# Kernel optimization log

Measured on AMD Instinct MI355X. Metric: run time of the kernel, lower is better.

Reference implementation:

```python
import jax, jax.numpy as jnp
import numpy as np

BETA = 1.0  # init beta


def l2norm(x, eps=1e-12):
    # matches torch F.normalize(dim=-1)
    n = jnp.sqrt(jnp.sum(x * x, axis=-1, keepdims=True))
    return x / jnp.maximum(n, eps)


def setup_inputs() -> dict:
    key = jax.random.key(0)
    k1, k2 = jax.random.split(key)
    B, T, D, N = 8, 2048, 256, 8192
    z = jax.random.normal(k1, (B, T, D), dtype=jnp.float32)
    # EMA codebook weight (buffer, not trained by grad); l2-normalized as the
    # norm-EMA update keeps it on the unit sphere.
    weight = l2norm(jax.random.normal(k2, (N, D), dtype=jnp.float32))
    return {"z": z, "weight": weight}


def reference(z, weight):
    # z: (B, T, D); weight: (N, D)
    z = l2norm(z)
    zf = z.reshape(-1, z.shape[-1])  # (BT, D)
    # squared L2 distances via expansion: |z|^2 + |w|^2 - 2 z.w
    d = (
        jnp.sum(zf * zf, axis=1, keepdims=True)
        + jnp.sum(weight * weight, axis=1)
        - 2.0 * jnp.einsum("bd,nd->bn", zf, weight)
    )  # (BT, N)
    encoding_indices = jnp.argmin(d, axis=1)  # (BT,)
    z_q = weight[encoding_indices].reshape(z.shape)  # (B, T, D)
    # commitment loss: beta * mse(stop_grad(z_q), z)
    loss = BETA * jnp.mean((jax.lax.stop_gradient(z_q) - z) ** 2)
    # straight-through estimator
    z_q = z + jax.lax.stop_gradient(z_q - z)
    encoding_indices = encoding_indices.reshape(z.shape[:-1])  # (B, T)
    return z_q, loss, encoding_indices
```

## Files before the change

### kernel.cpp

```cpp
#include <hip/hip_runtime.h>
#include <float.h>
#include <math.h>


#define BT_ 16384
#define D_  256
#define N_  8192
#define BETA_ 1.0f

#define BM 128
#define BN 256
#define NKT 8
#define NTILES 32

typedef __attribute__((ext_vector_type(8))) _Float16 f16x8;
typedef __attribute__((ext_vector_type(4))) float f32x4;

__device__ __forceinline__ void gld16(void* lds, const void* g) {
  __builtin_amdgcn_global_load_lds(
      (const __attribute__((address_space(1))) void*)g,
      (__attribute__((address_space(3))) void*)lds, 16, 0, 0);
}

__device__ __forceinline__ unsigned short f2h(float x) {
  _Float16 h = (_Float16)x;
  return __builtin_bit_cast(unsigned short, h);
}
__device__ __forceinline__ float h2f(unsigned short u) {
  return (float)__builtin_bit_cast(_Float16, u);
}
__device__ __forceinline__ unsigned ford(float f) {
  unsigned b = __float_as_uint(f);
  return (b & 0x80000000u) ? ~b : (b | 0x80000000u);
}

__global__ __launch_bounds__(256) void k_prep(const float* __restrict__ z,
                                              const float* __restrict__ w,
                                              float* __restrict__ zn,
                                              ushort* __restrict__ Acat,
                                              float* __restrict__ rl,
                                              float* __restrict__ wn2,
                                              ushort* __restrict__ Bcat) {
  const int b    = blockIdx.x;
  const int lane = threadIdx.x & 63;
  if (b < BT_ / 4) {
    const int row = b * 4 + (threadIdx.x >> 6);
    float4 v = *(reinterpret_cast<const float4*>(z) + (size_t)row * 64 + lane);
    float s = v.x * v.x + v.y * v.y + v.z * v.z + v.w * v.w;
#pragma unroll
    for (int o = 32; o > 0; o >>= 1) s += __shfl_xor(s, o, 64);
    float dn = fmaxf(sqrtf(s), 1e-12f);
    v.x /= dn; v.y /= dn; v.z /= dn; v.w /= dn;
    *(reinterpret_cast<float4*>(zn) + (size_t)row * 64 + lane) = v;
    ushort4 h = make_ushort4(f2h(v.x), f2h(v.y), f2h(v.z), f2h(v.w));
    float lx = v.x - h2f(h.x), ly = v.y - h2f(h.y);
    float lz = v.z - h2f(h.z), lw = v.w - h2f(h.w);
    float s2 = lx * lx + ly * ly + lz * lz + lw * lw;
#pragma unroll
    for (int o = 32; o > 0; o >>= 1) s2 += __shfl_xor(s2, o, 64);
    if (lane == 0) rl[row] = sqrtf(s2);
    reinterpret_cast<ushort4*>(Acat)[(size_t)row * 64 + lane] = h;
  } else {
    const int row = (b - BT_ / 4) * 4 + (threadIdx.x >> 6);
    float4 v = *(reinterpret_cast<const float4*>(w) + (size_t)row * 64 + lane);
    float s = v.x * v.x + v.y * v.y + v.z * v.z + v.w * v.w;
#pragma unroll
    for (int o = 32; o > 0; o >>= 1) s += __shfl_xor(s, o, 64);
    if (lane == 0) wn2[row] = s;
    ushort4 h  = make_ushort4(f2h(v.x), f2h(v.y), f2h(v.z), f2h(v.w));
    ushort4 lo = make_ushort4(f2h(v.x - h2f(h.x)), f2h(v.y - h2f(h.y)),
                              f2h(v.z - h2f(h.z)), f2h(v.w - h2f(h.w)));
    ushort4* B4 = reinterpret_cast<ushort4*>(Bcat);
    size_t rb = (size_t)row * 128 + lane;
    B4[rb]      = h;
    B4[rb + 64] = lo;
  }
}

__global__ __launch_bounds__(512, 4) void k_coarse(const ushort* __restrict__ Acat,
                                                   const ushort* __restrict__ Bcat,
                                                   const float* __restrict__ wn2,
                                                   float* __restrict__ tm,
                                                   float* __restrict__ ts,
                                                   int* __restrict__ ti,
                                                   float* __restrict__ tm2) {
  extern __shared__ char smem[];

  const int tid = threadIdx.x;
  const int l   = tid & 63;
  const int wv  = tid >> 6;
  const int wr  = wv >> 2;
  const int wc  = wv & 3;
  const int bid  = blockIdx.x;
  const int xcd  = bid & 7;
  const int q    = bid >> 3;
  const int chnk = q >> 5, wq = q & 31;
  const int rt   = xcd * 16 + (chnk >> 3) * 8 + (wq >> 2);
  const int ct   = (chnk & 7) * 4 + (wq & 3);
  const int row0 = rt * BM;
  const int col0 = ct * BN;

  const int sgr = ((l & 3) ^ ((l >> 3) & 3)) * 16;
  const char* gsrc[4];
  unsigned    ldst[4];
#pragma unroll
  for (int s = 0; s < 4; ++s) {
    int u = wv * 4 + s;
    gsrc[s] = (const char*)Bcat + (size_t)(col0 + (u & 15) * 16 + (l >> 2)) * 1024 +
              (u >> 4) * 512 + sgr;
    ldst[s] = u * 1024;
  }
#define STAGE(t)                                                               \
  do {                                                                         \
    char* _b = smem + ((t) & 1) * 32768;                                       \
    _Pragma("unroll")                                                          \
    for (int s = 0; s < 4; ++s) gld16(_b + ldst[s], gsrc[s] + (size_t)(t) * 64); \
  } while (0)

  const int lA = l & 15;
  const ushort* aB = Acat + (size_t)(row0 + wr * 64 + lA) * 256 + (l >> 4) * 8;
#define LOADA(t)                                                               \
  do {                                                                         \
    _Pragma("unroll")                                                          \
    for (int i = 0; i < 4; ++i)                                                \
      af[i] = *(const f16x8*)(aB + i * 4096 + (t) * 32);                       \
  } while (0)

  const int gk = (l >> 4) ^ ((lA >> 1) & 3);
  const unsigned bOff = (unsigned)((wc * 64 + lA) * 64 + gk * 16);

  f32x4 acc[4][4];
#pragma unroll
  for (int i = 0; i < 4; ++i)
#pragma unroll
    for (int j = 0; j < 4; ++j) acc[i][j] = (f32x4){0.f, 0.f, 0.f, 0.f};

  f16x8 af[4];
  STAGE(0);
  LOADA(0);

#pragma unroll
  for (int t = 0; t < NKT; ++t) {
    char* buf = smem + (t & 1) * 32768;
    asm volatile("s_waitcnt vmcnt(0)" ::: "memory");
    __builtin_amdgcn_s_barrier();
    __builtin_amdgcn_sched_barrier(0);
    if (t + 1 < NKT) STAGE(t + 1);

    f16x8 bg[4];
#pragma unroll
    for (int j = 0; j < 4; ++j)
      bg[j] = *(const f16x8*)(buf + bOff + j * 1024);
    __builtin_amdgcn_s_setprio(1);
#pragma unroll
    for (int i = 0; i < 4; ++i)
#pragma unroll
      for (int j = 0; j < 4; ++j)
        acc[i][j] = __builtin_amdgcn_mfma_f32_16x16x32_f16(af[i], bg[j], acc[i][j], 0, 0, 0);
    __builtin_amdgcn_s_setprio(0);
#pragma unroll
    for (int j = 0; j < 4; ++j)
      bg[j] = *(const f16x8*)(buf + 16384 + bOff + j * 1024);
    __builtin_amdgcn_s_setprio(1);
#pragma unroll
    for (int i = 0; i < 4; ++i)
#pragma unroll
      for (int j = 0; j < 4; ++j)
        acc[i][j] = __builtin_amdgcn_mfma_f32_16x16x32_f16(af[i], bg[j], acc[i][j], 0, 0, 0);
    __builtin_amdgcn_s_setprio(0);
    if (t + 1 < NKT) LOADA(t + 1);
  }
#undef STAGE
#undef LOADA

  float wnv[4];
#pragma unroll
  for (int n = 0; n < 4; ++n) wnv[n] = wn2[col0 + wc * 64 + n * 16 + lA];
  float* pm = (float*)smem;
  float* ps = (float*)(smem + 16896);
  int*   pc = (int*)(smem + 33792);
  __syncthreads();

#pragma unroll
  for (int i = 0; i < 4; ++i) {
#pragma unroll
    for (int qq = 0; qq < 4; ++qq) {
      float m = FLT_MAX, s = FLT_MAX; int c = 0;
#pragma unroll
      for (int j = 0; j < 4; ++j) {
        float d = fmaf(-2.0f, acc[i][j][qq], wnv[j]);
        int cc = wc * 64 + j * 16 + lA;
        if (d < m) { s = m; m = d; c = cc; }
        else if (d < s) s = d;
      }
      float om = __shfl_xor(m, 8, 64);
      float os = __shfl_xor(s, 8, 64);
      int   oc = __shfl_xor(c, 8, 64);
      float ns = fminf(fminf(s, os), fmaxf(m, om));
      if (om < m || (om == m && oc < c)) { m = om; c = oc; }
      s = ns;
      if ((l & 8) == 0) {
        int row = wr * 64 + i * 16 + (l >> 4) * 4 + qq;
        int w33 = row * 33 + wc * 8 + (l & 7);
        pm[w33] = m; ps[w33] = s; pc[w33] = c;
      }
    }
  }
  __syncthreads();
  {
    const int row = tid >> 2;
    const int qd  = tid & 3;
    float gm = FLT_MAX, gs = FLT_MAX; int gc = 0x7fffffff;
#pragma unroll
    for (int k = 0; k < 8; ++k) {
      int w33 = row * 33 + qd * 8 + k;
      float m = pm[w33], s = ps[w33]; int c = pc[w33];
      float ns = fminf(fminf(gs, s), fmaxf(gm, m));
      if (m < gm || (m == gm && c < gc)) { gm = m; gc = c; }
      gs = ns;
    }
    tm2[(size_t)(row0 + row) * 128 + ct * 4 + qd] = gm;
#pragma unroll
    for (int msk = 1; msk <= 2; msk <<= 1) {
      float om = __shfl_xor(gm, msk, 64);
      float os = __shfl_xor(gs, msk, 64);
      int   oc = __shfl_xor(gc, msk, 64);
      float ns = fminf(fminf(gs, os), fmaxf(gm, om));
      if (om < gm || (om == gm && oc < gc)) { gm = om; gc = oc; }
      gs = ns;
    }
    if (qd == 0) {
      size_t o = (size_t)ct * BT_ + row0 + row;
      tm[o] = gm; ts[o] = gs; ti[o] = col0 + gc;
    }
  }
}

__global__ __launch_bounds__(256) void k_combine(const float* __restrict__ tm,
                                                 const float* __restrict__ ts,
                                                 const int* __restrict__ ti,
                                                 const float* __restrict__ rl,
                                                 int* __restrict__ idxf,
                                                 float* __restrict__ lim,
                                                 unsigned long long* __restrict__ rowKey,
                                                 int* __restrict__ flagged,
                                                 int* __restrict__ count) {
  const int row = blockIdx.x * 256 + threadIdx.x;
  float m = FLT_MAX, s = FLT_MAX; int bi = 0x7fffffff;
#pragma unroll
  for (int t = 0; t < NTILES; ++t) {
    size_t o = (size_t)t * BT_ + row;
    float om = tm[o], os = ts[o]; int oi = ti[o];
    float nsv = fminf(fminf(s, os), fmaxf(m, om));
    if (om < m || (om == m && oi < bi)) { m = om; bi = oi; }
    s = nsv;
  }
  idxf[row] = bi;
  const float thr = 4.0f * rl[row] + 2.5e-4f;
  if (s - m <= thr) {
    rowKey[row] = ~0ULL;
    lim[row] = m + thr;
    int p = atomicAdd(count, 1);
    flagged[p] = row;
  } else {
    rowKey[row] = 0ULL;
  }
}

__global__ __launch_bounds__(256) void k_refine(const float* __restrict__ zn,
                                                const float* __restrict__ w,
                                                const float* __restrict__ wn2,
                                                const float* __restrict__ tm2,
                                                const float* __restrict__ lim,
                                                const int* __restrict__ flagged,
                                                const int* __restrict__ count,
                                                unsigned long long* __restrict__ rowKey) {
  __shared__ float4 znr[64];
  __shared__ int cand[128];
  __shared__ int ncand;
  const int tid = threadIdx.x;
  const int l   = tid & 63;
  const int wv  = tid >> 6;
  const int cnt = *count;
  for (int f = blockIdx.x; f < cnt; f += gridDim.x) {
    __syncthreads();
    const int row = flagged[f];
    if (tid == 0) ncand = 0;
    if (tid < 64)
      znr[tid] = *(reinterpret_cast<const float4*>(zn) + (size_t)row * 64 + tid);
    __syncthreads();
    const float lv = lim[row];
    if (tid < 128) {
      float t2 = tm2[(size_t)row * 128 + tid];
      if (t2 <= lv) { int p = atomicAdd(&ncand, 1); cand[p] = tid; }
    }
    __syncthreads();
    const int nc = ncand;
    unsigned long long key = ~0ULL;
    for (int i = wv; i < nc; i += 4) {
      const int g = cand[i];
      const int c = g * 64 + l;
      const float4* wr4 = reinterpret_cast<const float4*>(w) + (size_t)c * 64;
      float d0 = 0.f, d1 = 0.f, d2 = 0.f, d3 = 0.f;
#pragma unroll
      for (int k4 = 0; k4 < 16; ++k4) {
        float4 a0 = znr[k4 * 4 + 0], b0 = wr4[k4 * 4 + 0];
        float4 a1 = znr[k4 * 4 + 1], b1 = wr4[k4 * 4 + 1];
        float4 a2 = znr[k4 * 4 + 2], b2 = wr4[k4 * 4 + 2];
        float4 a3 = znr[k4 * 4 + 3], b3 = wr4[k4 * 4 + 3];
        d0 = fmaf(a0.x, b0.x, d0); d0 = fmaf(a0.y, b0.y, d0);
        d0 = fmaf(a0.z, b0.z, d0); d0 = fmaf(a0.w, b0.w, d0);
        d1 = fmaf(a1.x, b1.x, d1); d1 = fmaf(a1.y, b1.y, d1);
        d1 = fmaf(a1.z, b1.z, d1); d1 = fmaf(a1.w, b1.w, d1);
        d2 = fmaf(a2.x, b2.x, d2); d2 = fmaf(a2.y, b2.y, d2);
        d2 = fmaf(a2.z, b2.z, d2); d2 = fmaf(a2.w, b2.w, d2);
        d3 = fmaf(a3.x, b3.x, d3); d3 = fmaf(a3.y, b3.y, d3);
        d3 = fmaf(a3.z, b3.z, d3); d3 = fmaf(a3.w, b3.w, d3);
      }
      float dot = (d0 + d1) + (d2 + d3);
      float d = fmaf(-2.0f, dot, wn2[c]);
      unsigned long long k = ((unsigned long long)ford(d) << 32) | (unsigned)c;
      key = (k < key) ? k : key;
    }
#pragma unroll
    for (int msk = 1; msk < 64; msk <<= 1) {
      unsigned long long ok = __shfl_xor(key, msk, 64);
      key = (ok < key) ? ok : key;
    }
    if (l == 0 && key != ~0ULL) atomicMin(&rowKey[row], key);
  }
}

__global__ __launch_bounds__(256) void k_gather(const float* __restrict__ zn,
                                                const float* __restrict__ w,
                                                const int* __restrict__ idxf,
                                                const unsigned long long* __restrict__ rowKey,
                                                float* __restrict__ zq,
                                                float* __restrict__ idx_out,
                                                float* __restrict__ wpart) {
  const int row  = blockIdx.x * 4 + (threadIdx.x >> 6);
  const int lane = threadIdx.x & 63;
  unsigned long long key = rowKey[row];
  const int bi = (key == 0ULL) ? idxf[row] : (int)(key & 0xFFFFFFFFu);
  float4 cv = *(reinterpret_cast<const float4*>(w)  + (size_t)bi  * 64 + lane);
  float4 zv = *(reinterpret_cast<const float4*>(zn) + (size_t)row * 64 + lane);
  *(reinterpret_cast<float4*>(zq) + (size_t)row * 64 + lane) = cv;
  float dx = cv.x - zv.x, dy = cv.y - zv.y, dz = cv.z - zv.z, dw = cv.w - zv.w;
  float s = dx * dx + dy * dy + dz * dz + dw * dw;
#pragma unroll
  for (int o = 32; o > 0; o >>= 1) s += __shfl_xor(s, o, 64);
  if (lane == 0) {
    wpart[row] = s;
    idx_out[row] = (float)bi;
  }
}

__global__ __launch_bounds__(256) void k_final(const float* __restrict__ wpart,
                                               float* __restrict__ loss_out) {
  __shared__ float wsum[4];
  float s = 0.f;
  for (int i = threadIdx.x; i < BT_; i += 256) s += wpart[i];
#pragma unroll
  for (int o = 32; o > 0; o >>= 1) s += __shfl_xor(s, o, 64);
  if ((threadIdx.x & 63) == 0) wsum[threadIdx.x >> 6] = s;
  __syncthreads();
  if (threadIdx.x == 0)
    loss_out[0] = BETA_ * ((wsum[0] + wsum[1]) + (wsum[2] + wsum[3])) *
                  (1.0f / (float)(BT_ * D_));
}

extern "C" void kernel_launch(void* const* d_in, const int* in_sizes, int n_in,
                              void* d_out, int out_size, void* d_ws, size_t ws_size,
                              hipStream_t stream) {
  const float* z = (const float*)d_in[0];
  const float* w = (const float*)d_in[1];

  float* out      = (float*)d_out;
  float* zq       = out;
  float* loss_out = out + (size_t)BT_ * D_;
  float* idx_out  = loss_out + 1;

  char* wsb = (char*)d_ws;
  float*  zn      = (float*)(wsb);
  ushort* Acat    = (ushort*)(wsb + 16777216);
  ushort* Bcat    = (ushort*)(wsb + 25165824);
  float*  tm      = (float*)(wsb + 33554432);
  float*  ts      = (float*)(wsb + 37748736);
  int*    ti      = (int*)(wsb + 41943040);
  float*  tm2     = (float*)(wsb + 46137344);
  float*  wn2     = (float*)(wsb + 54525952);
  float*  rl      = (float*)(wsb + 54558720);
  int*    idxf    = (int*)(wsb + 54624256);
  float*  lim     = (float*)(wsb + 54689792);
  unsigned long long* rowKey = (unsigned long long*)(wsb + 54755328);
  int*    flagged = (int*)(wsb + 54886400);
  int*    count   = (int*)(wsb + 54951936);
  float*  wpart   = ts;

  hipFuncSetAttribute((const void*)k_coarse,
                      hipFuncAttributeMaxDynamicSharedMemorySize, 65536);

  hipMemsetAsync(count, 0, 4, stream);
  k_prep<<<BT_ / 4 + N_ / 4, 256, 0, stream>>>(z, w, zn, Acat, rl, wn2, Bcat);
  k_coarse<<<(BT_ / BM) * NTILES, 512, 65536, stream>>>(Acat, Bcat, wn2, tm, ts, ti, tm2);
  k_combine<<<BT_ / 256, 256, 0, stream>>>(tm, ts, ti, rl, idxf, lim, rowKey, flagged, count);
  k_refine<<<2048, 256, 0, stream>>>(zn, w, wn2, tm2, lim, flagged, count, rowKey);
  k_gather<<<BT_ / 4, 256, 0, stream>>>(zn, w, idxf, rowKey, zq, idx_out, wpart);
  k_final<<<1, 256, 0, stream>>>(wpart, loss_out);
}
```

Baseline: 293.5 us.

## Stage A tiles through LDS with async global-to-LDS loads in coarse GEMM

In the coarse distance GEMM, the A operand (normalized z in fp16) is now brought in with global_load_lds into a double-buffered LDS region, alongside the B tile. Previously each wave read its A fragments straight from global memory into registers. The copy work is spread over 5 load slots per wave, and fragments are read back from LDS with the same XOR swizzle used for B. The aim is to stop the four column-waves from fetching the same A rows redundantly from global memory and to move A into the existing async prefetch pipeline. In exchange, dynamic LDS grows from 64 KB to 80 KB, the main loop loses its unroll pragma, and the workspace offsets are repacked to match the actual buffer sizes.

```diff
diff --git a/kernel.cpp b/kernel.cpp
--- a/kernel.cpp
+++ b/kernel.cpp
@@ -101,33 +101,38 @@
   const int col0 = ct * BN;
 
   const int sgr = ((l & 3) ^ ((l >> 3) & 3)) * 16;
-  const char* gsrc[4];
-  unsigned    ldst[4];
-#pragma unroll
-  for (int s = 0; s < 4; ++s) {
-    int u = wv * 4 + s;
-    gsrc[s] = (const char*)Bcat + (size_t)(col0 + (u & 15) * 16 + (l >> 2)) * 1024 +
-              (u >> 4) * 512 + sgr;
-    ldst[s] = u * 1024;
+  const char* gsrc[5];
+  unsigned    base0[5];
+  unsigned    bstr[5];
+#pragma unroll
+  for (int s = 0; s < 5; ++s) {
+    int u = wv * 5 + s;
+    if (u < 8) {
+      gsrc[s]  = (const char*)Acat + (size_t)(row0 + u * 16 + (l >> 2)) * 512 + sgr;
+      base0[s] = u * 1024;
+      bstr[s]  = 8192;
+    } else if (u < 24) {
+      gsrc[s]  = (const char*)Bcat + (size_t)(col0 + (u - 8) * 16 + (l >> 2)) * 1024 + sgr;
+      base0[s] = 16384 + (u - 8) * 1024;
+      bstr[s]  = 32768;
+    } else {
+      gsrc[s]  = (const char*)Bcat + (size_t)(col0 + (u - 24) * 16 + (l >> 2)) * 1024 + 512 + sgr;
+      base0[s] = 16384 + 16384 + (u - 24) * 1024;
+      bstr[s]  = 32768;
+    }
   }
 #define STAGE(t)                                                               \
   do {                                                                         \
-    char* _b = smem + ((t) & 1) * 32768;                                       \
+    const unsigned _b = (unsigned)((t) & 1);                                   \
     _Pragma("unroll")                                                          \
-    for (int s = 0; s < 4; ++s) gld16(_b + ldst[s], gsrc[s] + (size_t)(t) * 64); \
+    for (int s = 0; s < 5; ++s)                                                \
+      gld16(smem + base0[s] + _b * bstr[s], gsrc[s] + (size_t)(t) * 64);       \
   } while (0)
 
-  const int lA = l & 15;
-  const ushort* aB = Acat + (size_t)(row0 + wr * 64 + lA) * 256 + (l >> 4) * 8;
-#define LOADA(t)                                                               \
-  do {                                                                         \
-    _Pragma("unroll")                                                          \
-    for (int i = 0; i < 4; ++i)                                                \
-      af[i] = *(const f16x8*)(aB + i * 4096 + (t) * 32);                       \
-  } while (0)
-
-  const int gk = (l >> 4) ^ ((lA >> 1) & 3);
-  const unsigned bOff = (unsigned)((wc * 64 + lA) * 64 + gk * 16);
+  const int lA  = l & 15;
+  const int gk  = (l >> 4) ^ ((lA >> 1) & 3);
+  const unsigned aOff  = (unsigned)((wr * 64 + lA) * 64 + gk * 16);
+  const unsigned bhOff = (unsigned)(16384 + (wc * 64 + lA) * 64 + gk * 16);
 
   f32x4 acc[4][4];
 #pragma unroll
@@ -135,22 +140,23 @@
 #pragma unroll
     for (int j = 0; j < 4; ++j) acc[i][j] = (f32x4){0.f, 0.f, 0.f, 0.f};
 
-  f16x8 af[4];
   STAGE(0);
-  LOADA(0);
-
-#pragma unroll
+
   for (int t = 0; t < NKT; ++t) {
-    char* buf = smem + (t & 1) * 32768;
+    const unsigned ab = (unsigned)((t & 1) * 8192);
+    const unsigned bb = (unsigned)((t & 1) * 32768);
     asm volatile("s_waitcnt vmcnt(0)" ::: "memory");
     __builtin_amdgcn_s_barrier();
     __builtin_amdgcn_sched_barrier(0);
     if (t + 1 < NKT) STAGE(t + 1);
 
-    f16x8 bg[4];
+    f16x8 af[4], bg[4];
+#pragma unroll
+    for (int i = 0; i < 4; ++i)
+      af[i] = *(const f16x8*)(smem + ab + aOff + i * 1024);
 #pragma unroll
     for (int j = 0; j < 4; ++j)
-      bg[j] = *(const f16x8*)(buf + bOff + j * 1024);
+      bg[j] = *(const f16x8*)(smem + bb + bhOff + j * 1024);
     __builtin_amdgcn_s_setprio(1);
 #pragma unroll
     for (int i = 0; i < 4; ++i)
@@ -160,7 +166,7 @@
     __builtin_amdgcn_s_setprio(0);
 #pragma unroll
     for (int j = 0; j < 4; ++j)
-      bg[j] = *(const f16x8*)(buf + 16384 + bOff + j * 1024);
+      bg[j] = *(const f16x8*)(smem + bb + bhOff + 16384 + j * 1024);
     __builtin_amdgcn_s_setprio(1);
 #pragma unroll
     for (int i = 0; i < 4; ++i)
@@ -168,10 +174,8 @@
       for (int j = 0; j < 4; ++j)
         acc[i][j] = __builtin_amdgcn_mfma_f32_16x16x32_f16(af[i], bg[j], acc[i][j], 0, 0, 0);
     __builtin_amdgcn_s_setprio(0);
-    if (t + 1 < NKT) LOADA(t + 1);
   }
 #undef STAGE
-#undef LOADA
 
   float wnv[4];
 #pragma unroll
@@ -385,24 +389,24 @@
   ushort* Acat    = (ushort*)(wsb + 16777216);
   ushort* Bcat    = (ushort*)(wsb + 25165824);
   float*  tm      = (float*)(wsb + 33554432);
-  float*  ts      = (float*)(wsb + 37748736);
-  int*    ti      = (int*)(wsb + 41943040);
-  float*  tm2     = (float*)(wsb + 46137344);
-  float*  wn2     = (float*)(wsb + 54525952);
-  float*  rl      = (float*)(wsb + 54558720);
-  int*    idxf    = (int*)(wsb + 54624256);
-  float*  lim     = (float*)(wsb + 54689792);
-  unsigned long long* rowKey = (unsigned long long*)(wsb + 54755328);
-  int*    flagged = (int*)(wsb + 54886400);
-  int*    count   = (int*)(wsb + 54951936);
+  float*  ts      = (float*)(wsb + 35651584);
+  int*    ti      = (int*)(wsb + 37748736);
+  float*  tm2     = (float*)(wsb + 39845888);
+  float*  wn2     = (float*)(wsb + 48234496);
+  float*  rl      = (float*)(wsb + 48267264);
+  int*    idxf    = (int*)(wsb + 48331328);
+  float*  lim     = (float*)(wsb + 48396864);
+  unsigned long long* rowKey = (unsigned long long*)(wsb + 48462400);
+  int*    flagged = (int*)(wsb + 48593472);
+  int*    count   = (int*)(wsb + 48659008);
   float*  wpart   = ts;
 
   hipFuncSetAttribute((const void*)k_coarse,
-                      hipFuncAttributeMaxDynamicSharedMemorySize, 65536);
+                      hipFuncAttributeMaxDynamicSharedMemorySize, 81920);
 
   hipMemsetAsync(count, 0, 4, stream);
   k_prep<<<BT_ / 4 + N_ / 4, 256, 0, stream>>>(z, w, zn, Acat, rl, wn2, Bcat);
-  k_coarse<<<(BT_ / BM) * NTILES, 512, 65536, stream>>>(Acat, Bcat, wn2, tm, ts, ti, tm2);
+  k_coarse<<<(BT_ / BM) * NTILES, 512, 81920, stream>>>(Acat, Bcat, wn2, tm, ts, ti, tm2);
   k_combine<<<BT_ / 256, 256, 0, stream>>>(tm, ts, ti, rl, idxf, lim, rowKey, flagged, count);
   k_refine<<<2048, 256, 0, stream>>>(zn, w, wn2, tm2, lim, flagged, count, rowKey);
   k_gather<<<BT_ / 4, 256, 0, stream>>>(zn, w, idxf, rowKey, zq, idx_out, wpart);
```

New measurement: 240.3 us. -18.1%, faster.
